# Kernel optimization log

Measured on AMD Instinct MI355X. Metric: run time of the kernel, lower is better.

The kernel has to match this reference:

```python
import jax, jax.numpy as jnp
import numpy as np
from jax import lax

FAULT_RATE = 0.1


def _quant_inject(key, x, num_faults):
    # scale/zero-point quantization to [0,255] (matches compute_scale_zero_point)
    mn, mx = x.min(), x.max()
    scale = (mx - mn) / 255.0
    zp = jnp.clip(-mn / scale, 0.0, 255.0)
    q = jnp.clip(jnp.round(zp + x / scale), 0.0, 255.0)
    if num_faults > 0:
        # vectorized equivalent of the serial fault loop: pick unique indices,
        # each consumes a random 1..8 fault budget; faulted bytes are zeroed
        # (the original loop sets tensor_bits = 0).
        n = q.size
        m = min(num_faults, n)  # each index consumes >= 1 fault
        k1, k2 = jax.random.split(key)
        cand = jax.random.permutation(k1, n)[:m]  # without replacement
        sizes = jax.random.randint(k2, (m,), 1, 9)
        prefix = jnp.cumsum(sizes) - sizes  # budget consumed before each pick
        keep = prefix < num_faults
        qf = q.reshape(-1)
        qf = qf.at[cand].set(jnp.where(keep, jnp.zeros((), q.dtype), qf[cand]))
        q = qf.reshape(q.shape)
    return scale * (q - zp)


def _conv(x, w, b):
    y = lax.conv_general_dilated(x, w, (1, 1), 'VALID',
                                 dimension_numbers=('NCHW', 'OIHW', 'NCHW'))
    return y + b[None, :, None, None]


def _maxpool(x):
    return lax.reduce_window(x, -np.inf, lax.max, (1, 1, 2, 2), (1, 1, 2, 2), 'VALID')


def _fault_schedule(total_activation_count):
    total_faults = int(total_activation_count * 8 * FAULT_RATE)
    rng = np.random.default_rng(0)
    return [int(v) for v in rng.multinomial(total_faults, np.ones(4) / 4)]


def _forward(x, conv1_w, conv1_b, conv2_w, conv2_b, fc_w, fc_b,
             fc1_w, fc1_b, fc2_w, fc2_b, fpl):
    ks = jax.random.split(jax.random.key(42), 11)
    x = _conv(x, conv1_w, conv1_b)
    x = _quant_inject(ks[0], x, 0)
    x = jax.nn.relu(x)
    x = _quant_inject(ks[1], x, fpl[0])
    x = _maxpool(x)
    x = _quant_inject(ks[2], x, 0)
    x = _conv(x, conv2_w, conv2_b)
    x = _quant_inject(ks[3], x, 0)
    x = jax.nn.relu(x)
    x = _quant_inject(ks[4], x, fpl[1])
    x = _maxpool(x)
    x = _quant_inject(ks[5], x, 0)
    x = x.reshape(x.shape[0], -1)  # [B, 400]
    x = x @ fc_w.T + fc_b
    x = _quant_inject(ks[6], x, 0)
    x = jax.nn.relu(x)
    x = _quant_inject(ks[7], x, fpl[2])
    x = x @ fc1_w.T + fc1_b
    x = _quant_inject(ks[8], x, 0)
    x = jax.nn.relu(x)
    x = _quant_inject(ks[9], x, fpl[3])
    x = x @ fc2_w.T + fc2_b
    x = _quant_inject(ks[10], x, 0)
    return jax.nn.log_softmax(x, axis=1)


def setup_inputs() -> dict:
    key = jax.random.key(0)
    ks = jax.random.split(key, 11)
    B = 8192
    return {
        'x': jax.random.normal(ks[0], (B, 1, 32, 32), jnp.float32),
        'conv1_w': jax.random.normal(ks[1], (6, 1, 5, 5), jnp.float32) * 0.2,
        'conv1_b': jax.random.normal(ks[2], (6,), jnp.float32) * 0.1,
        'conv2_w': jax.random.normal(ks[3], (16, 6, 5, 5), jnp.float32) * 0.08,
        'conv2_b': jax.random.normal(ks[4], (16,), jnp.float32) * 0.1,
        'fc_w': jax.random.normal(ks[5], (120, 400), jnp.float32) * 0.05,
        'fc_b': jax.random.normal(ks[6], (120,), jnp.float32) * 0.1,
        'fc1_w': jax.random.normal(ks[7], (84, 120), jnp.float32) * 0.09,
        'fc1_b': jax.random.normal(ks[8], (84,), jnp.float32) * 0.1,
        'fc2_w': jax.random.normal(ks[9], (10, 84), jnp.float32) * 0.1,
        'fc2_b': jax.random.normal(ks[10], (10,), jnp.float32) * 0.1,
        'total_activation_count': 833024,
    }


def reference(x, conv1_w, conv1_b, conv2_w, conv2_b, fc_w, fc_b,
              fc1_w, fc1_b, fc2_w, fc2_b, total_activation_count):
    fpl = _fault_schedule(total_activation_count)
    return _forward(x, conv1_w, conv1_b, conv2_w, conv2_b, fc_w, fc_b,
                    fc1_w, fc1_b, fc2_w, fc2_b, fpl)
```

## Files before the change

kernel.cpp:

```cpp
#include <hip/hip_runtime.h>
#include <cstdint>
#include <cstring>
#include <cmath>
#include <cstdlib>
#include <vector>
#include <thread>
#include <mutex>
#include <algorithm>

#define JAX_PARTITIONABLE 1


static inline uint32_t rotl32(uint32_t v, int d) { return (v << d) | (v >> (32 - d)); }

static inline void tf2x32(uint32_t k0, uint32_t k1, uint32_t c0, uint32_t c1,
                          uint32_t& o0, uint32_t& o1) {
  uint32_t ks0 = k0, ks1 = k1, ks2 = k0 ^ k1 ^ 0x1BD11BDAu;
  uint32_t ks[3] = {ks0, ks1, ks2};
  uint32_t x0 = c0 + ks0, x1 = c1 + ks1;
  static const int R[2][4] = {{13, 15, 26, 6}, {17, 29, 16, 24}};
  for (int g = 0; g < 5; g++) {
    const int* r = R[g & 1];
    for (int q = 0; q < 4; q++) { x0 += x1; x1 = rotl32(x1, r[q]); x1 ^= x0; }
    x0 += ks[(g + 1) % 3];
    x1 += ks[(g + 2) % 3] + (uint32_t)(g + 1);
  }
  o0 = x0; o1 = x1;
}

static void jax_split(const uint32_t key[2], int num, uint32_t (*out)[2]) {
#if JAX_PARTITIONABLE
  for (int i = 0; i < num; i++)
    tf2x32(key[0], key[1], 0u, (uint32_t)i, out[i][0], out[i][1]);
#else
  std::vector<uint32_t> o(2 * (size_t)num);
  for (int i = 0; i < num; i++) {
    uint32_t a, b;
    tf2x32(key[0], key[1], (uint32_t)i, (uint32_t)(num + i), a, b);
    o[i] = a; o[num + i] = b;
  }
  for (int i = 0; i < num; i++) { out[i][0] = o[2 * i]; out[i][1] = o[2 * i + 1]; }
#endif
}

static inline uint32_t jax_bits32_at(const uint32_t key[2], uint64_t n_total, uint64_t i) {
#if JAX_PARTITIONABLE
  uint32_t b0, b1;
  tf2x32(key[0], key[1], (uint32_t)(i >> 32), (uint32_t)i, b0, b1);
  return b0 ^ b1;
#else
  uint64_t half = (n_total + 1) / 2;
  uint64_t pi = (i < half) ? i : (i - half);
  uint32_t c1 = (half + pi < n_total) ? (uint32_t)(half + pi) : 0u;
  uint32_t b0, b1;
  tf2x32(key[0], key[1], (uint32_t)pi, c1, b0, b1);
  return (i < half) ? b0 : b1;
#endif
}

static void seedseq_zero_state(uint64_t out[4]) {
  const uint32_t INIT_A = 0x43b0d7e5u, MULT_A = 0x931e8875u;
  const uint32_t INIT_B = 0x8b51f9ddu, MULT_B = 0x58f38dedu;
  uint32_t pool[4];
  uint32_t hc = INIT_A;
  auto hashmix = [&](uint32_t v) -> uint32_t {
    v ^= hc; hc *= MULT_A; v *= hc; v ^= v >> 16; return v;
  };
  auto mixf = [](uint32_t x, uint32_t y) -> uint32_t {
    uint32_t r = x * 0xca01f9ddu - y * 0x4973f715u;
    r ^= r >> 16; return r;
  };
  uint32_t entropy0 = 0u;
  for (int i = 0; i < 4; i++) pool[i] = hashmix(i < 1 ? entropy0 : 0u);
  for (int s = 0; s < 4; s++)
    for (int d = 0; d < 4; d++)
      if (s != d) pool[d] = mixf(pool[d], hashmix(pool[s]));
  uint32_t st[8];
  uint32_t hc2 = INIT_B;
  int cyc = 0;
  for (int i = 0; i < 8; i++) {
    uint32_t v = pool[cyc]; cyc = (cyc + 1) & 3;
    v ^= hc2; hc2 *= MULT_B; v *= hc2; v ^= v >> 16;
    st[i] = v;
  }
  for (int k = 0; k < 4; k++)
    out[k] = (uint64_t)st[2 * k] | ((uint64_t)st[2 * k + 1] << 32);
}

struct PCG64 {
  __uint128_t state, inc;
  explicit PCG64(const uint64_t s[4]) {
    __uint128_t initstate = (((__uint128_t)s[0]) << 64) | s[1];
    __uint128_t initseq = (((__uint128_t)s[2]) << 64) | s[3];
    state = 0; inc = (initseq << 1) | 1;
    step(); state += initstate; step();
  }
  void step() {
    const __uint128_t MUL =
        (((__uint128_t)0x2360ed051fc65da4ULL) << 64) | 0x4385df649fccf645ULL;
    state = state * MUL + inc;
  }
  uint64_t next64() {
    step();
    uint64_t hi = (uint64_t)(state >> 64), lo = (uint64_t)state;
    uint64_t x = hi ^ lo;
    unsigned rot = (unsigned)(state >> 122);
    return (x >> rot) | (x << ((64u - rot) & 63u));
  }
  double nextd() { return (double)(next64() >> 11) * (1.0 / 9007199254740992.0); }
};

static int64_t binomial_inversion(PCG64& st, int64_t n, double p) {
  double q = 1.0 - p;
  double qn = std::exp(n * std::log(q));
  double np_ = n * p;
  int64_t bound = (int64_t)std::min((double)n, np_ + 10.0 * std::sqrt(np_ * q + 1));
  int64_t X = 0;
  double px = qn;
  double U = st.nextd();
  while (U > px) {
    X++;
    if (X > bound) { X = 0; px = qn; U = st.nextd(); }
    else { U -= px; px = ((n - X + 1) * p * px) / (X * q); }
  }
  return X;
}

static int64_t random_binomial_btpe(PCG64& st, int64_t n, double p) {
  double r, q, fm, p1, xm, xl, xr, c, laml, lamr, p2, p3, p4;
  double a, u, v, s, F, rho, t, A, nrq, x1, x2, f1, f2, z, z2, w, w2, x;
  int64_t m, y, k, i;
  r = std::min(p, 1.0 - p);
  q = 1.0 - r;
  fm = n * r + r;
  m = (int64_t)std::floor(fm);
  p1 = std::floor(2.195 * std::sqrt(n * r * q) - 4.6 * q) + 0.5;
  xm = m + 0.5;
  xl = xm - p1;
  xr = xm + p1;
  c = 0.134 + 20.5 / (15.3 + m);
  a = (fm - xl) / (fm - xl * r);
  laml = a * (1.0 + a / 2.0);
  a = (xr - fm) / (xr * q);
  lamr = a * (1.0 + a / 2.0);
  p2 = p1 * (1.0 + 2.0 * c);
  p3 = p2 + c / laml;
  p4 = p3 + c / lamr;

Step10:
  nrq = n * r * q;
  u = st.nextd() * p4;
  v = st.nextd();
  if (u > p1) goto Step20;
  y = (int64_t)std::floor(xm - p1 * v + u);
  goto Step60;
Step20:
  if (u > p2) goto Step30;
  x = xl + (u - p1) / c;
  v = v * c + 1.0 - std::fabs(m - x + 0.5) / p1;
  if (v > 1.0) goto Step10;
  y = (int64_t)std::floor(x);
  goto Step50;
Step30:
  if (u > p3) goto Step40;
  y = (int64_t)std::floor(xl + std::log(v) / laml);
  if ((y < 0) || (v == 0.0)) goto Step10;
  v = v * (u - p2) * laml;
  goto Step50;
Step40:
  y = (int64_t)std::floor(xr - std::log(v) / lamr);
  if ((y > n) || (v == 0.0)) goto Step10;
  v = v * (u - p3) * lamr;
  goto Step50;
Step50:
  k = (y > m) ? (y - m) : (m - y);
  if ((k > 20) && (k < (nrq / 2.0 - 1))) goto Step52;
  s = r / q;
  a = s * (n + 1);
  F = 1.0;
  if (m < y) { for (i = m + 1; i <= y; i++) F *= (a / i - s); }
  else if (m > y) { for (i = y + 1; i <= m; i++) F /= (a / i - s); }
  if (v > F) goto Step10;
  goto Step60;
Step52:
  rho = ((double)k / nrq) * ((k * (k / 3.0 + 0.625) + 0.16666666666666666) / nrq + 0.5);
  t = -((double)k) * k / (2 * nrq);
  A = std::log(v);
  if (A < (t - rho)) goto Step60;
  if (A > (t + rho)) goto Step10;
  x1 = (double)(y + 1);
  f1 = (double)(m + 1);
  z = (double)(n + 1 - m);
  w = (double)(n - y + 1);
  x2 = x1 * x1; f2 = f1 * f1; z2 = z * z; w2 = w * w;
  if (A > (xm * std::log(f1 / x1) + (n - m + 0.5) * std::log(z / w) +
           (y - m) * std::log(w * r / (x1 * q)) +
           (13680. - (462. - (132. - (99. - 140. / f2) / f2) / f2) / f2) / f1 / 166320. +
           (13680. - (462. - (132. - (99. - 140. / z2) / z2) / z2) / z2) / z / 166320. +
           (13680. - (462. - (132. - (99. - 140. / x2) / x2) / x2) / x2) / x1 / 166320. +
           (13680. - (462. - (132. - (99. - 140. / w2) / w2) / w2) / w2) / w / 166320.)) {
    goto Step10;
  }
Step60:
  if (p > 0.5) y = n - y;
  return y;
}

static int64_t random_binomial(PCG64& st, double p, int64_t n) {
  if (n == 0 || p == 0.0) return 0;
  if (p <= 0.5) {
    if (p * n <= 30.0) return binomial_inversion(st, n, p);
    return random_binomial_btpe(st, n, p);
  } else {
    double q = 1.0 - p;
    if (q * n <= 30.0) return n - binomial_inversion(st, n, q);
    return n - random_binomial_btpe(st, n, q);
  }
}

static void np_multinomial4(int64_t n, int64_t out[4]) {
  uint64_t ss[4];
  seedseq_zero_state(ss);
  PCG64 st(ss);
  double pix[4] = {0.25, 0.25, 0.25, 0.25};
  double remaining_p = 1.0;
  int64_t dn = n;
  out[0] = out[1] = out[2] = out[3] = 0;
  for (int j = 0; j < 3; j++) {
    out[j] = random_binomial(st, pix[j] / remaining_p, dn);
    dn -= out[j];
    if (dn <= 0) break;
    remaining_p -= pix[j];
  }
  if (dn > 0) out[3] = dn;
}

template <typename F>
static void pfor(size_t n, int T, const F& f) {
  if (n == 0) return;
  size_t chunk = (n + (size_t)T - 1) / (size_t)T;
  std::vector<std::thread> ths;
  for (int t = 0; t < T; t++) {
    size_t lo = (size_t)t * chunk;
    if (lo >= n) break;
    size_t hi = std::min(n, lo + chunk);
    ths.emplace_back([&f, lo, hi, t]() { f(lo, hi, t); });
  }
  for (auto& th : ths) th.join();
}

static void radix_pass16(const uint32_t* kin, const uint32_t* vin, uint32_t* kout,
                         uint32_t* vout, size_t n, int shift, int T,
                         std::vector<uint32_t>& hist) {
  const size_t BN = 65536;
  hist.assign((size_t)T * BN, 0u);
  pfor(n, T, [&](size_t lo, size_t hi, int t) {
    uint32_t* h = &hist[(size_t)t * BN];
    for (size_t i = lo; i < hi; i++) h[(kin[i] >> shift) & 0xFFFFu]++;
  });
  uint32_t sum = 0;
  for (size_t d = 0; d < BN; d++)
    for (int t = 0; t < T; t++) {
      uint32_t& hc = hist[(size_t)t * BN + d];
      uint32_t cnt = hc; hc = sum; sum += cnt;
    }
  pfor(n, T, [&](size_t lo, size_t hi, int t) {
    uint32_t* h = &hist[(size_t)t * BN];
    for (size_t i = lo; i < hi; i++) {
      uint32_t d = (kin[i] >> shift) & 0xFFFFu;
      uint32_t pos = h[d]++;
      kout[pos] = kin[i]; vout[pos] = vin[i];
    }
  });
}

static void shuffle_prefix(const uint32_t key[2], uint64_t n, uint32_t J,
                           uint32_t* out, int T) {
  if (J == 0) return;
  double nn = (double)(n < 1 ? 1 : n);
  int rounds = (int)std::ceil(3.0 * std::log(nn) / std::log(4294967295.0));
  size_t N = (size_t)n;
  std::vector<uint32_t> kbuf(N), vbuf(N), kt(N), vt(N);
  std::vector<uint32_t> hist;
  pfor(N, T, [&](size_t lo, size_t hi, int) {
    for (size_t i = lo; i < hi; i++) vbuf[i] = (uint32_t)i;
  });
  uint32_t cur[2] = {key[0], key[1]};
  for (int rd = 0; rd < rounds; rd++) {
    uint32_t ch[2][2];
    jax_split(cur, 2, ch);
    cur[0] = ch[0][0]; cur[1] = ch[0][1];
    uint32_t sk[2] = {ch[1][0], ch[1][1]};
#if JAX_PARTITIONABLE
    pfor(N, T, [&](size_t lo, size_t hi, int) {
      for (size_t i = lo; i < hi; i++) {
        uint32_t b0, b1;
        tf2x32(sk[0], sk[1], (uint32_t)(i >> 32), (uint32_t)i, b0, b1);
        kbuf[i] = b0 ^ b1;
      }
    });
#else
    {
      size_t half = (N + 1) / 2;
      pfor(half, T, [&](size_t lo, size_t hi, int) {
        for (size_t i = lo; i < hi; i++) {
          uint32_t c1v = (half + i < N) ? (uint32_t)(half + i) : 0u;
          uint32_t b0, b1;
          tf2x32(sk[0], sk[1], (uint32_t)i, c1v, b0, b1);
          kbuf[i] = b0;
          if (half + i < N) kbuf[half + i] = b1;
        }
      });
    }
#endif
    radix_pass16(kbuf.data(), vbuf.data(), kt.data(), vt.data(), N, 0, T, hist);
    radix_pass16(kt.data(), vt.data(), kbuf.data(), vbuf.data(), N, 16, T, hist);
  }
  for (uint32_t j = 0; j < J; j++) out[j] = vbuf[j];
  std::sort(out, out + J);
}


static uint32_t h_faults[4 * 65536];
static uint32_t h_blob[64 + 4 * 65536];
static int h_J[4] = {0, 0, 0, 0};
static int h_off[4] = {0, 0, 0, 0};
static int h_tot = 0;
static uint64_t h_tables_B = 0;

static void compute_fault_tables(uint64_t B, int Jout[4]) {
  int T = (int)std::thread::hardware_concurrency();
  if (T < 1) T = 1;
  if (T > 48) T = 48;
  int64_t fpl[4];
  np_multinomial4((int64_t)(833024ull * 8ull / 10ull), fpl);
  uint32_t k42[2] = {0u, 42u};
  uint32_t ks[11][2];
  jax_split(k42, 11, ks);
  const int kidx[4] = {1, 4, 7, 9};
  const uint64_t ns[4] = {B * 4704u, B * 1600u, B * 120u, B * 84u};
  for (int L = 0; L < 4; L++) {
    uint32_t ch[2][2];
    jax_split(ks[kidx[L]], 2, ch);
    uint32_t rc[2][2];
    jax_split(ch[1], 2, rc);
    int64_t nf = fpl[L];
    uint64_t m = ((uint64_t)nf < ns[L]) ? (uint64_t)nf : ns[L];
    int64_t csum = 0;
    uint32_t J = 0;
    for (uint64_t j = 0; j < m; j++) {
      if (csum >= nf) break;
      J++;
      csum += 1 + (int64_t)(jax_bits32_at(rc[1], m, j) & 7u);
    }
    if (J > 65536u) J = 65536u;
    shuffle_prefix(ch[0], ns[L], J, &h_faults[(size_t)L * 65536], T);
    Jout[L] = (int)J;
  }
  memset(h_blob, 0, 256);
  for (int s = 0; s < 11; s++) { h_blob[2 * s] = 0xFFFFFFFFu; h_blob[2 * s + 1] = 0u; }
  int tot = 0;
  for (int L = 0; L < 4; L++) {
    h_off[L] = tot;
    memcpy(h_blob + 64 + tot, h_faults + (size_t)L * 65536, (size_t)Jout[L] * 4);
    tot += Jout[L];
  }
  h_tot = tot;
}

namespace {
struct FaultTableInit {
  FaultTableInit() {
    compute_fault_tables(8192ull, h_J);
    h_tables_B = 8192ull;
  }
};
FaultTableInit g_fault_table_init;
std::mutex g_table_mu;
}


#define INF_F __builtin_inff()

__device__ __forceinline__ uint32_t f_to_mono(float f) {
  uint32_t u = __float_as_uint(f);
  return (u & 0x80000000u) ? ~u : (u | 0x80000000u);
}
__device__ __forceinline__ float mono_to_f(uint32_t m) {
  uint32_t u = (m & 0x80000000u) ? (m & 0x7FFFFFFFu) : ~m;
  return __uint_as_float(u);
}

struct QP { float scale; float zp; };

__device__ __forceinline__ QP qp_make(float mn, float mx) {
  QP p;
  p.scale = (mx - mn) / 255.0f;
  p.zp = fminf(fmaxf((-mn) / p.scale, 0.0f), 255.0f);
  return p;
}
__device__ __forceinline__ QP qp_load(const uint32_t* stats, int s) {
  return qp_make(mono_to_f(stats[2 * s + 0]), mono_to_f(stats[2 * s + 1]));
}
__device__ __forceinline__ float quant_apply(float x, QP p) {
  float q = rintf(p.zp + x / p.scale);
  q = fminf(fmaxf(q, 0.0f), 255.0f);
  return p.scale * (q - p.zp);
}
__device__ __forceinline__ float quant_zero(QP p) { return p.scale * (0.0f - p.zp); }
__device__ __forceinline__ int q_idx(float x, QP p) {
  float q = rintf(p.zp + x / p.scale);
  q = fminf(fmaxf(q, 0.0f), 255.0f);
  return (int)q;
}

__device__ __forceinline__ QP qp_derive_relu(const uint32_t* stats, int s, QP qa) {
  float mn = mono_to_f(stats[2 * s + 0]);
  float mx = mono_to_f(stats[2 * s + 1]);
  float dmn = fmaxf(quant_apply(mn, qa), 0.0f);
  float dmx = fmaxf(quant_apply(mx, qa), 0.0f);
  return qp_make(dmn, dmx);
}

__device__ __forceinline__ void block_minmax(float lmn, float lmx, uint32_t* mn_slot,
                                             uint32_t* mx_slot) {
  for (int off = 32; off > 0; off >>= 1) {
    lmn = fminf(lmn, __shfl_down(lmn, off, 64));
    lmx = fmaxf(lmx, __shfl_down(lmx, off, 64));
  }
  __shared__ float wmn[16], wmx[16];
  int wid = threadIdx.x >> 6, lane = threadIdx.x & 63;
  int nw = (blockDim.x + 63) >> 6;
  if (lane == 0) { wmn[wid] = lmn; wmx[wid] = lmx; }
  __syncthreads();
  if (threadIdx.x == 0) {
    float m0 = wmn[0], m1 = wmx[0];
    for (int i = 1; i < nw; i++) { m0 = fminf(m0, wmn[i]); m1 = fmaxf(m1, wmx[i]); }
    atomicMin(mn_slot, f_to_mono(m0));
    atomicMax(mx_slot, f_to_mono(m1));
  }
}

__device__ __forceinline__ int lowb(const uint32_t* a, int n, uint32_t v) {
  int lo = 0, hi = n;
  while (lo < hi) {
    int mid = (lo + hi) >> 1;
    if (a[mid] < v) lo = mid + 1; else hi = mid;
  }
  return lo;
}


template <int IMG>
__device__ __forceinline__ void stage_img(const float* __restrict__ x, float* s_img,
                                          int ib0, int B) {
  for (int i = threadIdx.x; i < IMG * 256; i += 256) {
    int im = i >> 8, k = i & 255;
    if (ib0 + im < B) {
      float4 v = ((const float4*)(x + (size_t)(ib0 + im) * 1024))[k];
      int row = k >> 3, c4 = k & 7;
      ((float4*)s_img)[im * 288 + row * 9 + c4] = v;
    }
  }
}

__device__ __forceinline__ void stage_w1(const float* __restrict__ w, float* s_w) {
  if (threadIdx.x < 168) {
    int c = threadIdx.x / 28, f = threadIdx.x - c * 28;
    s_w[threadIdx.x] = (f < 25) ? w[c * 25 + f] : 0.0f;
  }
}

template <int O>
__device__ __forceinline__ void conv1_rowpair(const float* __restrict__ img, int r0,
                                              int colbase, const float* wr,
                                              float acc0[14], float acc1[14]) {
#pragma unroll
  for (int ir = 0; ir < 6; ir++) {
    float f[20];
    const float* rp = img + (r0 + ir) * 36 + colbase;
#pragma unroll
    for (int k = 0; k < 5; k++) *(float4*)&f[4 * k] = *(const float4*)&rp[4 * k];
    if (ir < 5) {
#pragma unroll
      for (int j = 0; j < 5; j++)
#pragma unroll
        for (int cc = 0; cc < 14; cc++)
          acc0[cc] = fmaf(f[O + cc + j], wr[ir * 5 + j], acc0[cc]);
    }
    if (ir >= 1) {
#pragma unroll
      for (int j = 0; j < 5; j++)
#pragma unroll
        for (int cc = 0; cc < 14; cc++)
          acc1[cc] = fmaf(f[O + cc + j], wr[(ir - 1) * 5 + j], acc1[cc]);
    }
  }
}

__global__ __launch_bounds__(256) void k_conv1_mat(const float* __restrict__ x,
    const float* __restrict__ w, const float* __restrict__ b,
    float* __restrict__ raw, uint32_t* __restrict__ stats, int B) {
  __shared__ __align__(16) float s_img[4 * 1152];
  __shared__ __align__(16) float s_w[168];
  __shared__ float s_b[8];
  int ib0 = blockIdx.x * 4;
  stage_img<4>(x, s_img, ib0, B);
  stage_w1(w, s_w);
  if (threadIdx.x < 6) s_b[threadIdx.x] = b[threadIdx.x];
  __syncthreads();
  float lmn = INF_F, lmx = -INF_F;
#pragma unroll 1
  for (int task = threadIdx.x; task < 4 * 168; task += 256) {
    int im = task / 168, rem = task - im * 168;
    if (ib0 + im >= B) continue;
    int c = rem / 28, r2 = rem - c * 28, pr = r2 >> 1, h = r2 & 1;
    float wr[25];
#pragma unroll
    for (int k = 0; k < 25; k++) wr[k] = s_w[c * 28 + k];
    float bias = s_b[c];
    float acc0[14], acc1[14];
#pragma unroll
    for (int cc = 0; cc < 14; cc++) { acc0[cc] = bias; acc1[cc] = bias; }
    const float* img = &s_img[im * 1152];
    if (h == 0) conv1_rowpair<0>(img, 2 * pr, 0, wr, acc0, acc1);
    else        conv1_rowpair<2>(img, 2 * pr, 12, wr, acc0, acc1);
    float* d0 = raw + (size_t)(ib0 + im) * 4704 + c * 784 + (2 * pr) * 28 + h * 14;
    float* d1 = d0 + 28;
#pragma unroll
    for (int q = 0; q < 7; q++) {
      float2 v0; v0.x = acc0[2 * q]; v0.y = acc0[2 * q + 1];
      float2 v1; v1.x = acc1[2 * q]; v1.y = acc1[2 * q + 1];
      *(float2*)&d0[2 * q] = v0;
      *(float2*)&d1[2 * q] = v1;
    }
#pragma unroll
    for (int cc = 0; cc < 14; cc++) {
      lmn = fminf(lmn, fminf(acc0[cc], acc1[cc]));
      lmx = fmaxf(lmx, fmaxf(acc0[cc], acc1[cc]));
    }
  }
  block_minmax(lmn, lmx, &stats[0], &stats[1]);
}

__global__ __launch_bounds__(256) void k_pool1(const float* __restrict__ raw,
    uint32_t* __restrict__ stats, const uint32_t* __restrict__ faults, int J,
    float* __restrict__ p1, int B) {
  __shared__ float s_K[256];
  __shared__ uint32_t s_fl[64];
  __shared__ int s_lo, s_nf;
  QP q0 = qp_load(stats, 0);
  QP qB = qp_derive_relu(stats, 0, q0);
  {
    int i = threadIdx.x;
    float a = fmaxf(q0.scale * ((float)i - q0.zp), 0.0f);
    float kq = rintf(qB.zp + a / qB.scale);
    s_K[i] = fminf(fmaxf(kq, 0.0f), 255.0f);
  }
  int T0 = blockIdx.x * 256;
  if (threadIdx.x == 0) {
    int im0 = T0 / 84;
    int imL = (T0 + 255) / 84;
    uint32_t lo32 = (uint32_t)im0 * 4704u;
    uint32_t hi32 = (uint32_t)(imL + 1) * 4704u;
    int lo = lowb(faults, J, lo32);
    s_lo = lo; s_nf = lowb(faults, J, hi32) - lo;
  }
  __syncthreads();
  int nf = s_nf, flo = s_lo;
  for (int i = threadIdx.x; i < nf && i < 64; i += 256) s_fl[i] = faults[flo + i];
  __syncthreads();
  const uint32_t* farr = (nf <= 64) ? s_fl : (faults + flo);

  float lmn = INF_F, lmx = -INF_F;
  int T = T0 + threadIdx.x;
  if (T < B * 84) {
    int im = T / 84, rem = T - im * 84;
    int c = rem / 14, pr = rem - c * 14;
    uint32_t e0 = (uint32_t)im * 4704u + (uint32_t)(c * 784 + 2 * pr * 28);
    const float* src = raw + (size_t)im * 4704 + c * 784 + (2 * pr) * 28;
    float k0[28], k1[28];
#pragma unroll
    for (int q = 0; q < 7; q++) {
      float4 v = *(const float4*)&src[4 * q];
      k0[4 * q + 0] = s_K[q_idx(v.x, q0)];
      k0[4 * q + 1] = s_K[q_idx(v.y, q0)];
      k0[4 * q + 2] = s_K[q_idx(v.z, q0)];
      k0[4 * q + 3] = s_K[q_idx(v.w, q0)];
    }
#pragma unroll
    for (int q = 0; q < 7; q++) {
      float4 v = *(const float4*)&src[28 + 4 * q];
      k1[4 * q + 0] = s_K[q_idx(v.x, q0)];
      k1[4 * q + 1] = s_K[q_idx(v.y, q0)];
      k1[4 * q + 2] = s_K[q_idx(v.z, q0)];
      k1[4 * q + 3] = s_K[q_idx(v.w, q0)];
    }
    if (nf > 0) {
      int a = lowb(farr, nf, e0);
      while (a < nf) {
        uint32_t g = farr[a];
        if (g >= e0 + 56u) break;
        int d = (int)(g - e0);
#pragma unroll
        for (int cc = 0; cc < 28; cc++) {
          if (cc == d) k0[cc] = 0.0f;
          if (cc + 28 == d) k1[cc] = 0.0f;
        }
        a++;
      }
    }
    float* dst = p1 + (size_t)im * 1176 + c * 196 + pr * 14;
#pragma unroll
    for (int q = 0; q < 7; q++) {
      float ka = fmaxf(fmaxf(k0[4 * q], k0[4 * q + 1]), fmaxf(k1[4 * q], k1[4 * q + 1]));
      float kb = fmaxf(fmaxf(k0[4 * q + 2], k0[4 * q + 3]),
                       fmaxf(k1[4 * q + 2], k1[4 * q + 3]));
      float2 v;
      v.x = qB.scale * (ka - qB.zp);
      v.y = qB.scale * (kb - qB.zp);
      *(float2*)&dst[2 * q] = v;
      lmn = fminf(lmn, fminf(v.x, v.y));
      lmx = fmaxf(lmx, fmaxf(v.x, v.y));
    }
  }
  block_minmax(lmn, lmx, &stats[4], &stats[5]);
}

__global__ __launch_bounds__(256) void k_conv2(const float* __restrict__ p1,
    const float* __restrict__ w, const float* __restrict__ b,
    float* __restrict__ raw, uint32_t* __restrict__ stats, int B) {
  __shared__ __align__(16) float s_in[8 * 1680];
  __shared__ __align__(16) float s_w[16 * 6 * 28];
  __shared__ float s_b[16];
  int ib0 = blockIdx.x * 8;
  QP q2 = qp_load(stats, 2);
  for (int i = threadIdx.x; i < 8 * 1176; i += 256) {
    int im = i / 1176, rem = i - im * 1176;
    if (ib0 + im < B) {
      int ci = rem / 196, r2 = rem - ci * 196;
      int rr = r2 / 14, cc = r2 - rr * 14;
      float v = quant_apply(p1[(size_t)(ib0 + im) * 1176 + rem], q2);
      s_in[im * 1680 + ci * 280 + rr * 20 + cc] = v;
    }
  }
  for (int i = threadIdx.x; i < 2688; i += 256) {
    int fi = i / 28, f = i - fi * 28;
    s_w[i] = (f < 25) ? w[fi * 25 + f] : 0.0f;
  }
  if (threadIdx.x < 16) s_b[threadIdx.x] = b[threadIdx.x];
  __syncthreads();
  float lmn = INF_F, lmx = -INF_F;
#pragma unroll 1
  for (int task = threadIdx.x; task < 640; task += 256) {
    int im = task / 80, rem = task - im * 80;
    if (ib0 + im >= B) continue;
    int c2p = rem / 10, r = rem - c2p * 10;
    int cA = 2 * c2p, cB = 2 * c2p + 1;
    float accA[10], accB[10];
    float bA = s_b[cA], bB = s_b[cB];
#pragma unroll
    for (int cc = 0; cc < 10; cc++) { accA[cc] = bA; accB[cc] = bB; }
    const float* inb = &s_in[im * 1680];
#pragma unroll 1
    for (int ci = 0; ci < 6; ci++) {
      float wrA[28], wrB[28];
#pragma unroll
      for (int k = 0; k < 7; k++) {
        *(float4*)&wrA[4 * k] = *(const float4*)&s_w[(cA * 6 + ci) * 28 + 4 * k];
        *(float4*)&wrB[4 * k] = *(const float4*)&s_w[(cB * 6 + ci) * 28 + 4 * k];
      }
      const float* cb = inb + ci * 280;
#pragma unroll
      for (int i = 0; i < 5; i++) {
        float f[16];
        const float* rp = cb + (r + i) * 20;
#pragma unroll
        for (int k = 0; k < 4; k++) *(float4*)&f[4 * k] = *(const float4*)&rp[4 * k];
#pragma unroll
        for (int j = 0; j < 5; j++) {
#pragma unroll
          for (int cc = 0; cc < 10; cc++) accA[cc] = fmaf(f[cc + j], wrA[i * 5 + j], accA[cc]);
#pragma unroll
          for (int cc = 0; cc < 10; cc++) accB[cc] = fmaf(f[cc + j], wrB[i * 5 + j], accB[cc]);
        }
      }
    }
    float* rbA = raw + (size_t)(ib0 + im) * 1600 + cA * 100 + r * 10;
    float* rbB = raw + (size_t)(ib0 + im) * 1600 + cB * 100 + r * 10;
#pragma unroll
    for (int cc = 0; cc < 10; cc++) {
      rbA[cc] = accA[cc]; rbB[cc] = accB[cc];
      lmn = fminf(lmn, fminf(accA[cc], accB[cc]));
      lmx = fmaxf(lmx, fmaxf(accA[cc], accB[cc]));
    }
  }
  block_minmax(lmn, lmx, &stats[6], &stats[7]);
}

__global__ __launch_bounds__(256) void k_pool2s(const float* __restrict__ raw,
    uint32_t* __restrict__ stats, const uint32_t* __restrict__ faults, int J,
    float* __restrict__ p2, int B) {
  __shared__ float s_K[256];
  __shared__ uint32_t s_fl[64];
  __shared__ int s_lo, s_nf;
  QP q3 = qp_load(stats, 3);
  QP qE = qp_derive_relu(stats, 3, q3);
  {
    int i = threadIdx.x;
    float a = fmaxf(q3.scale * ((float)i - q3.zp), 0.0f);
    float kq = rintf(qE.zp + a / qE.scale);
    s_K[i] = fminf(fmaxf(kq, 0.0f), 255.0f);
  }
  int T0 = blockIdx.x * 256;
  if (threadIdx.x == 0) {
    int im0 = T0 / 80;
    int imL = (T0 + 255) / 80;
    uint32_t lo32 = (uint32_t)im0 * 1600u;
    uint32_t hi32 = (uint32_t)(imL + 1) * 1600u;
    int lo = lowb(faults, J, lo32);
    s_lo = lo; s_nf = lowb(faults, J, hi32) - lo;
  }
  __syncthreads();
  int nf = s_nf, flo = s_lo;
  for (int i = threadIdx.x; i < nf && i < 64; i += 256) s_fl[i] = faults[flo + i];
  __syncthreads();
  const uint32_t* farr = (nf <= 64) ? s_fl : (faults + flo);

  float lmn = INF_F, lmx = -INF_F;
  int T = T0 + threadIdx.x;
  if (T < B * 80) {
    int im = T / 80, rem = T - im * 80;
    int c = rem / 5, pr = rem - c * 5;
    uint32_t e0 = (uint32_t)im * 1600u + (uint32_t)(c * 100 + 2 * pr * 10);
    const float* src = raw + (size_t)im * 1600 + c * 100 + (2 * pr) * 10;
    float kk[20];
#pragma unroll
    for (int q = 0; q < 5; q++) {
      float4 v = *(const float4*)&src[4 * q];
      kk[4 * q + 0] = s_K[q_idx(v.x, q3)];
      kk[4 * q + 1] = s_K[q_idx(v.y, q3)];
      kk[4 * q + 2] = s_K[q_idx(v.z, q3)];
      kk[4 * q + 3] = s_K[q_idx(v.w, q3)];
    }
    if (nf > 0) {
      int a = lowb(farr, nf, e0);
      while (a < nf) {
        uint32_t g = farr[a];
        if (g >= e0 + 20u) break;
        int d = (int)(g - e0);
#pragma unroll
        for (int cc = 0; cc < 20; cc++) if (cc == d) kk[cc] = 0.0f;
        a++;
      }
    }
    float* dst = p2 + (size_t)im * 400 + c * 25 + pr * 5;
#pragma unroll
    for (int q = 0; q < 5; q++) {
      float kp = fmaxf(fmaxf(kk[2 * q], kk[2 * q + 1]),
                       fmaxf(kk[10 + 2 * q], kk[10 + 2 * q + 1]));
      float v = qE.scale * (kp - qE.zp);
      dst[q] = v;
      lmn = fminf(lmn, v); lmx = fmaxf(lmx, v);
    }
  }
  block_minmax(lmn, lmx, &stats[10], &stats[11]);
}

template <int IN, int OUT, int ROWS, int SPLIT, bool CHAIN>
__global__ __launch_bounds__(256) void k_fc(const float* __restrict__ in,
    const float* __restrict__ w, const float* __restrict__ bias,
    float* __restrict__ out, uint32_t* stats, int squant, int s_out,
    const uint32_t* __restrict__ faults, int J) {
  __shared__ __align__(16) float rows[ROWS * IN];
  int b0 = blockIdx.x * ROWS;
  QP p{1.0f, 0.0f};
  if (CHAIN) {
    QP qa = qp_load(stats, squant);
    p = qp_derive_relu(stats, squant, qa);
    for (int i = threadIdx.x; i < ROWS * IN; i += 256)
      rows[i] = quant_apply(fmaxf(quant_apply(in[(size_t)b0 * IN + i], qa), 0.0f), p);
  } else {
    p = qp_load(stats, squant);
    for (int i = threadIdx.x; i < ROWS * IN; i += 256)
      rows[i] = quant_apply(in[(size_t)b0 * IN + i], p);
  }
  if (faults) {
    __syncthreads();
    uint32_t base = (uint32_t)b0 * IN;
    int lo = lowb(faults, J, base), hi2 = lowb(faults, J, base + ROWS * IN);
    float qz = quant_zero(p);
    for (int t = lo + (int)threadIdx.x; t < hi2; t += 256) rows[faults[t] - base] = qz;
  }
  __syncthreads();
  constexpr int RP = ROWS / SPLIT;
  int o = threadIdx.x % OUT;
  int sp = threadIdx.x / OUT;
  float lmn = INF_F, lmx = -INF_F;
  if (sp < SPLIT) {
    float acc[RP];
#pragma unroll
    for (int r = 0; r < RP; r++) acc[r] = bias[o];
    const float* wr = &w[(size_t)o * IN];
    for (int k = 0; k < IN; k += 4) {
      float4 wv = *(const float4*)&wr[k];
#pragma unroll
      for (int r = 0; r < RP; r++) {
        float4 xv = *(const float4*)&rows[(sp * RP + r) * IN + k];
        acc[r] = fmaf(xv.x, wv.x, acc[r]);
        acc[r] = fmaf(xv.y, wv.y, acc[r]);
        acc[r] = fmaf(xv.z, wv.z, acc[r]);
        acc[r] = fmaf(xv.w, wv.w, acc[r]);
      }
    }
#pragma unroll
    for (int r = 0; r < RP; r++) {
      out[(size_t)(b0 + sp * RP + r) * OUT + o] = acc[r];
      lmn = fminf(lmn, acc[r]); lmx = fmaxf(lmx, acc[r]);
    }
  }
  block_minmax(lmn, lmx, &stats[2 * s_out], &stats[2 * s_out + 1]);
}

__global__ __launch_bounds__(256) void k_logsoftmax(const float* __restrict__ logits,
    float* __restrict__ out, const uint32_t* stats, int slot, int B) {
  int i = blockIdx.x * 256 + threadIdx.x;
  if (i >= B) return;
  QP p = qp_load(stats, slot);
  float v[10];
  float m = -INF_F;
#pragma unroll
  for (int k = 0; k < 10; k++) {
    v[k] = quant_apply(logits[(size_t)i * 10 + k], p);
    m = fmaxf(m, v[k]);
  }
  float s = 0.0f;
#pragma unroll
  for (int k = 0; k < 10; k++) s += expf(v[k] - m);
  float ls = logf(s);
#pragma unroll
  for (int k = 0; k < 10; k++) out[(size_t)i * 10 + k] = (v[k] - m) - ls;
}

extern "C" void kernel_launch(void* const* d_in, const int* in_sizes, int n_in,
                              void* d_out, int out_size, void* d_ws, size_t ws_size,
                              hipStream_t stream) {
  const float* x    = (const float*)d_in[0];
  const float* c1w  = (const float*)d_in[1];
  const float* c1b  = (const float*)d_in[2];
  const float* c2w  = (const float*)d_in[3];
  const float* c2b  = (const float*)d_in[4];
  const float* fcw  = (const float*)d_in[5];
  const float* fcb  = (const float*)d_in[6];
  const float* fc1w = (const float*)d_in[7];
  const float* fc1b = (const float*)d_in[8];
  const float* fc2w = (const float*)d_in[9];
  const float* fc2b = (const float*)d_in[10];
  float* out = (float*)d_out;
  const int B = in_sizes[0] / 1024;

  if ((uint64_t)B != h_tables_B) {
    std::lock_guard<std::mutex> lk(g_table_mu);
    if ((uint64_t)B != h_tables_B) {
      compute_fault_tables((uint64_t)B, h_J);
      h_tables_B = (uint64_t)B;
    }
  }

  uint8_t* ws = (uint8_t*)d_ws;
  uint32_t* stats = (uint32_t*)ws;
  uint32_t* fl = (uint32_t*)(ws + 256);
  size_t off = 256 + (size_t)4 * 65536 * sizeof(uint32_t);
  float* p1   = (float*)(ws + off); off += (size_t)B * 1176 * 4;
  float* p2   = (float*)(ws + off); off += (size_t)B * 400 * 4;
  float* h1   = (float*)(ws + off); off += (size_t)B * 120 * 4;
  float* h2   = (float*)(ws + off); off += (size_t)B * 84 * 4;
  float* lg   = (float*)(ws + off); off += (size_t)B * 10 * 4;
  float* raw2 = (float*)(ws + off); off += (size_t)B * 1600 * 4;
  float* raw1 = (float*)(ws + off); off += (size_t)B * 4704 * 4;
  if (ws_size < off) return;

  const uint32_t* f0 = fl + h_off[0];
  const uint32_t* f1 = fl + h_off[1];
  const uint32_t* f2 = fl + h_off[2];
  const uint32_t* f3 = fl + h_off[3];

  hipMemcpyAsync(ws, h_blob, 256 + (size_t)h_tot * sizeof(uint32_t),
                 hipMemcpyHostToDevice, stream);

  int g4 = (B + 3) / 4, g8 = (B + 7) / 8;

  k_conv1_mat<<<g4, 256, 0, stream>>>(x, c1w, c1b, raw1, stats, B);
  k_pool1<<<(B * 84 + 255) / 256, 256, 0, stream>>>(raw1, stats, f0, h_J[0], p1, B);

  k_conv2<<<g8, 256, 0, stream>>>(p1, c2w, c2b, raw2, stats, B);
  k_pool2s<<<(B * 80 + 255) / 256, 256, 0, stream>>>(raw2, stats, f1, h_J[1], p2, B);

  k_fc<400, 120, 16, 2, false><<<B / 16, 256, 0, stream>>>(p2, fcw, fcb, h1, stats,
                                                           5, 6, nullptr, 0);
  k_fc<120, 84, 16, 2, true><<<B / 16, 256, 0, stream>>>(h1, fc1w, fc1b, h2, stats,
                                                         6, 8, f2, h_J[2]);
  k_fc<84, 10, 32, 8, true><<<B / 32, 256, 0, stream>>>(h2, fc2w, fc2b, lg, stats,
                                                        8, 10, f3, h_J[3]);
  k_logsoftmax<<<(B + 255) / 256, 256, 0, stream>>>(lg, out, stats, 10, B);
}
```

Before: 614.1 us.

## Fuse 2x2 window max into conv1 and store only faulted windows in full

Result: no change. 623.4 us (+1.5%).

```diff
diff --git a/kernel.cpp b/kernel.cpp
--- a/kernel.cpp
+++ b/kernel.cpp
@@ -322,10 +322,11 @@
 
 
 static uint32_t h_faults[4 * 65536];
-static uint32_t h_blob[64 + 4 * 65536];
+static uint32_t h_blob[64 + 5 * 65536];
 static int h_J[4] = {0, 0, 0, 0};
 static int h_off[4] = {0, 0, 0, 0};
 static int h_tot = 0;
+static int h_nfw = 0;
 static uint64_t h_tables_B = 0;
 
 static void compute_fault_tables(uint64_t B, int Jout[4]) {
@@ -366,6 +367,21 @@
     tot += Jout[L];
   }
   h_tot = tot;
+  {
+    std::vector<uint32_t> wv;
+    wv.reserve(Jout[0]);
+    for (int j = 0; j < Jout[0]; j++) {
+      uint32_t e = h_faults[j];
+      uint32_t im = e / 4704u, rem = e - im * 4704u;
+      uint32_t c = rem / 784u, r2 = rem - c * 784u;
+      uint32_t rr = r2 / 28u, cc = r2 - rr * 28u;
+      wv.push_back(im * 1176u + c * 196u + (rr >> 1) * 14u + (cc >> 1));
+    }
+    std::sort(wv.begin(), wv.end());
+    wv.erase(std::unique(wv.begin(), wv.end()), wv.end());
+    h_nfw = (int)std::min<size_t>(wv.size(), 65536);
+    memcpy(h_blob + 64 + tot, wv.data(), (size_t)h_nfw * 4);
+  }
 }
 
 namespace {
@@ -459,7 +475,7 @@
     if (ib0 + im < B) {
       float4 v = ((const float4*)(x + (size_t)(ib0 + im) * 1024))[k];
       int row = k >> 3, c4 = k & 7;
-      ((float4*)s_img)[im * 288 + row * 9 + c4] = v;
+      ((float4*)s_img)[im * 320 + row * 10 + c4] = v;
     }
   }
 }
@@ -478,7 +494,7 @@
 #pragma unroll
   for (int ir = 0; ir < 6; ir++) {
     float f[20];
-    const float* rp = img + (r0 + ir) * 36 + colbase;
+    const float* rp = img + (r0 + ir) * 40 + colbase;
 #pragma unroll
     for (int k = 0; k < 5; k++) *(float4*)&f[4 * k] = *(const float4*)&rp[4 * k];
     if (ir < 5) {
@@ -500,15 +516,30 @@
 
 __global__ __launch_bounds__(256) void k_conv1_mat(const float* __restrict__ x,
     const float* __restrict__ w, const float* __restrict__ b,
-    float* __restrict__ raw, uint32_t* __restrict__ stats, int B) {
-  __shared__ __align__(16) float s_img[4 * 1152];
+    float* __restrict__ wmax, float* __restrict__ side,
+    const uint32_t* __restrict__ fw, int nfw_g,
+    uint32_t* __restrict__ stats, int B) {
+  __shared__ __align__(16) float s_img[4 * 1280];
   __shared__ __align__(16) float s_w[168];
   __shared__ float s_b[8];
+  __shared__ uint32_t s_fw[64];
+  __shared__ int s_flo, s_fn;
   int ib0 = blockIdx.x * 4;
   stage_img<4>(x, s_img, ib0, B);
   stage_w1(w, s_w);
   if (threadIdx.x < 6) s_b[threadIdx.x] = b[threadIdx.x];
+  if (threadIdx.x == 0) {
+    uint32_t w0 = (uint32_t)ib0 * 1176u;
+    uint32_t w1 = (uint32_t)(ib0 + 4) * 1176u;
+    int lo = lowb(fw, nfw_g, w0);
+    s_flo = lo; s_fn = lowb(fw, nfw_g, w1) - lo;
+  }
   __syncthreads();
+  int fn = s_fn, flo = s_flo;
+  for (int i = threadIdx.x; i < fn && i < 64; i += 256) s_fw[i] = fw[flo + i];
+  __syncthreads();
+  const uint32_t* fwa = (fn <= 64) ? s_fw : (fw + flo);
+
   float lmn = INF_F, lmx = -INF_F;
 #pragma unroll 1
   for (int task = threadIdx.x; task < 4 * 168; task += 256) {
@@ -522,17 +553,33 @@
     float acc0[14], acc1[14];
 #pragma unroll
     for (int cc = 0; cc < 14; cc++) { acc0[cc] = bias; acc1[cc] = bias; }
-    const float* img = &s_img[im * 1152];
+    const float* img = &s_img[im * 1280];
     if (h == 0) conv1_rowpair<0>(img, 2 * pr, 0, wr, acc0, acc1);
     else        conv1_rowpair<2>(img, 2 * pr, 12, wr, acc0, acc1);
-    float* d0 = raw + (size_t)(ib0 + im) * 4704 + c * 784 + (2 * pr) * 28 + h * 14;
-    float* d1 = d0 + 28;
-#pragma unroll
-    for (int q = 0; q < 7; q++) {
-      float2 v0; v0.x = acc0[2 * q]; v0.y = acc0[2 * q + 1];
-      float2 v1; v1.x = acc1[2 * q]; v1.y = acc1[2 * q + 1];
-      *(float2*)&d0[2 * q] = v0;
-      *(float2*)&d1[2 * q] = v1;
+    uint32_t wid0 = (uint32_t)(ib0 + im) * 1176u + (uint32_t)(c * 196 + pr * 14 + h * 7);
+    float* dst = wmax + wid0;
+#pragma unroll
+    for (int k = 0; k < 7; k++) {
+      float wm = fmaxf(fmaxf(acc0[2 * k], acc0[2 * k + 1]),
+                       fmaxf(acc1[2 * k], acc1[2 * k + 1]));
+      dst[k] = wm;
+    }
+    if (fn > 0) {
+      int a = lowb(fwa, fn, wid0);
+      while (a < fn) {
+        uint32_t wg = fwa[a];
+        if (wg >= wid0 + 7u) break;
+#pragma unroll
+        for (int k = 0; k < 7; k++) {
+          if ((int)(wg - wid0) == k) {
+            float4 sv;
+            sv.x = acc0[2 * k]; sv.y = acc0[2 * k + 1];
+            sv.z = acc1[2 * k]; sv.w = acc1[2 * k + 1];
+            *(float4*)&side[4 * (flo + a)] = sv;
+          }
+        }
+        a++;
+      }
     }
 #pragma unroll
     for (int cc = 0; cc < 14; cc++) {
@@ -543,85 +590,85 @@
   block_minmax(lmn, lmx, &stats[0], &stats[1]);
 }
 
-__global__ __launch_bounds__(256) void k_pool1(const float* __restrict__ raw,
-    uint32_t* __restrict__ stats, const uint32_t* __restrict__ faults, int J,
-    float* __restrict__ p1, int B) {
-  __shared__ float s_K[256];
-  __shared__ uint32_t s_fl[64];
-  __shared__ int s_lo, s_nf;
+__global__ __launch_bounds__(256) void k_pool1(const float* __restrict__ wmax,
+    const float* __restrict__ side, const uint32_t* __restrict__ fw, int nfw_g,
+    const uint32_t* __restrict__ faults, int J,
+    uint32_t* __restrict__ stats, float* __restrict__ p1, int B) {
+  __shared__ float s_V[256];
+  __shared__ uint32_t s_fw[64], s_fl[64];
+  __shared__ int s_wlo, s_wn, s_elo, s_en;
   QP q0 = qp_load(stats, 0);
   QP qB = qp_derive_relu(stats, 0, q0);
   {
     int i = threadIdx.x;
     float a = fmaxf(q0.scale * ((float)i - q0.zp), 0.0f);
-    float kq = rintf(qB.zp + a / qB.scale);
-    s_K[i] = fminf(fmaxf(kq, 0.0f), 255.0f);
+    float kq = fminf(fmaxf(rintf(qB.zp + a / qB.scale), 0.0f), 255.0f);
+    s_V[i] = qB.scale * (kq - qB.zp);
   }
   int T0 = blockIdx.x * 256;
   if (threadIdx.x == 0) {
-    int im0 = T0 / 84;
-    int imL = (T0 + 255) / 84;
-    uint32_t lo32 = (uint32_t)im0 * 4704u;
-    uint32_t hi32 = (uint32_t)(imL + 1) * 4704u;
-    int lo = lowb(faults, J, lo32);
-    s_lo = lo; s_nf = lowb(faults, J, hi32) - lo;
+    int im0 = T0 / 84, imL = (T0 + 255) / 84;
+    uint32_t w0 = (uint32_t)im0 * 1176u, w1 = (uint32_t)(imL + 1) * 1176u;
+    int lo = lowb(fw, nfw_g, w0);
+    s_wlo = lo; s_wn = lowb(fw, nfw_g, w1) - lo;
+    uint32_t e0 = (uint32_t)im0 * 4704u, e1 = (uint32_t)(imL + 1) * 4704u;
+    int lo2 = lowb(faults, J, e0);
+    s_elo = lo2; s_en = lowb(faults, J, e1) - lo2;
   }
   __syncthreads();
-  int nf = s_nf, flo = s_lo;
-  for (int i = threadIdx.x; i < nf && i < 64; i += 256) s_fl[i] = faults[flo + i];
+  int wn = s_wn, wlo = s_wlo, en = s_en, elo = s_elo;
+  for (int i = threadIdx.x; i < wn && i < 64; i += 256) s_fw[i] = fw[wlo + i];
+  for (int i = threadIdx.x; i < en && i < 64; i += 256) s_fl[i] = faults[elo + i];
   __syncthreads();
-  const uint32_t* farr = (nf <= 64) ? s_fl : (faults + flo);
+  const uint32_t* fwa = (wn <= 64) ? s_fw : (fw + wlo);
+  const uint32_t* fla = (en <= 64) ? s_fl : (faults + elo);
 
   float lmn = INF_F, lmx = -INF_F;
   int T = T0 + threadIdx.x;
   if (T < B * 84) {
     int im = T / 84, rem = T - im * 84;
     int c = rem / 14, pr = rem - c * 14;
-    uint32_t e0 = (uint32_t)im * 4704u + (uint32_t)(c * 784 + 2 * pr * 28);
-    const float* src = raw + (size_t)im * 4704 + c * 784 + (2 * pr) * 28;
-    float k0[28], k1[28];
+    uint32_t rb = (uint32_t)im * 1176u + (uint32_t)(c * 196 + pr * 14);
+    const float* src = wmax + rb;
+    float v[14];
 #pragma unroll
     for (int q = 0; q < 7; q++) {
-      float4 v = *(const float4*)&src[4 * q];
-      k0[4 * q + 0] = s_K[q_idx(v.x, q0)];
-      k0[4 * q + 1] = s_K[q_idx(v.y, q0)];
-      k0[4 * q + 2] = s_K[q_idx(v.z, q0)];
-      k0[4 * q + 3] = s_K[q_idx(v.w, q0)];
-    }
-#pragma unroll
-    for (int q = 0; q < 7; q++) {
-      float4 v = *(const float4*)&src[28 + 4 * q];
-      k1[4 * q + 0] = s_K[q_idx(v.x, q0)];
-      k1[4 * q + 1] = s_K[q_idx(v.y, q0)];
-      k1[4 * q + 2] = s_K[q_idx(v.z, q0)];
-      k1[4 * q + 3] = s_K[q_idx(v.w, q0)];
-    }
-    if (nf > 0) {
-      int a = lowb(farr, nf, e0);
-      while (a < nf) {
-        uint32_t g = farr[a];
-        if (g >= e0 + 56u) break;
-        int d = (int)(g - e0);
-#pragma unroll
-        for (int cc = 0; cc < 28; cc++) {
-          if (cc == d) k0[cc] = 0.0f;
-          if (cc + 28 == d) k1[cc] = 0.0f;
-        }
+      float2 wm = *(const float2*)&src[2 * q];
+      v[2 * q]     = s_V[q_idx(wm.x, q0)];
+      v[2 * q + 1] = s_V[q_idx(wm.y, q0)];
+    }
+    if (wn > 0) {
+      int a = lowb(fwa, wn, rb);
+      while (a < wn) {
+        uint32_t wg = fwa[a];
+        if (wg >= rb + 14u) break;
+        int wc = (int)(wg - rb);
+        float4 sv = *(const float4*)&side[4 * (wlo + a)];
+        uint32_t eb = (uint32_t)im * 4704u + (uint32_t)(c * 784 + 2 * pr * 28 + 2 * wc);
+        float m0, mm = 0.0f;
+        int p2_;
+        p2_ = lowb(fla, en, eb);       m0 = (p2_ < en && fla[p2_] == eb)       ? 0.0f : (float)q_idx(sv.x, q0);
+        mm = fmaxf(mm * 0.0f, m0);
+        p2_ = lowb(fla, en, eb + 1u);  m0 = (p2_ < en && fla[p2_] == eb + 1u)  ? 0.0f : (float)q_idx(sv.y, q0);
+        mm = fmaxf(mm, m0);
+        p2_ = lowb(fla, en, eb + 28u); m0 = (p2_ < en && fla[p2_] == eb + 28u) ? 0.0f : (float)q_idx(sv.z, q0);
+        mm = fmaxf(mm, m0);
+        p2_ = lowb(fla, en, eb + 29u); m0 = (p2_ < en && fla[p2_] == eb + 29u) ? 0.0f : (float)q_idx(sv.w, q0);
+        mm = fmaxf(mm, m0);
+        float aa = fmaxf(q0.scale * (mm - q0.zp), 0.0f);
+        float kq = fminf(fmaxf(rintf(qB.zp + aa / qB.scale), 0.0f), 255.0f);
+#pragma unroll
+        for (int k = 0; k < 14; k++) if (k == wc) v[k] = qB.scale * (kq - qB.zp);
         a++;
       }
     }
-    float* dst = p1 + (size_t)im * 1176 + c * 196 + pr * 14;
+    float* dst = p1 + rb;
 #pragma unroll
     for (int q = 0; q < 7; q++) {
-      float ka = fmaxf(fmaxf(k0[4 * q], k0[4 * q + 1]), fmaxf(k1[4 * q], k1[4 * q + 1]));
-      float kb = fmaxf(fmaxf(k0[4 * q + 2], k0[4 * q + 3]),
-                       fmaxf(k1[4 * q + 2], k1[4 * q + 3]));
-      float2 v;
-      v.x = qB.scale * (ka - qB.zp);
-      v.y = qB.scale * (kb - qB.zp);
-      *(float2*)&dst[2 * q] = v;
-      lmn = fminf(lmn, fminf(v.x, v.y));
-      lmx = fmaxf(lmx, fmaxf(v.x, v.y));
+      float2 o; o.x = v[2 * q]; o.y = v[2 * q + 1];
+      *(float2*)&dst[2 * q] = o;
+      lmn = fminf(lmn, fminf(o.x, o.y));
+      lmx = fmaxf(lmx, fmaxf(o.x, o.y));
     }
   }
   block_minmax(lmn, lmx, &stats[4], &stats[5]);
@@ -870,28 +917,31 @@
   uint8_t* ws = (uint8_t*)d_ws;
   uint32_t* stats = (uint32_t*)ws;
   uint32_t* fl = (uint32_t*)(ws + 256);
-  size_t off = 256 + (size_t)4 * 65536 * sizeof(uint32_t);
+  size_t off = 256 + (size_t)5 * 65536 * sizeof(uint32_t);
   float* p1   = (float*)(ws + off); off += (size_t)B * 1176 * 4;
   float* p2   = (float*)(ws + off); off += (size_t)B * 400 * 4;
   float* h1   = (float*)(ws + off); off += (size_t)B * 120 * 4;
   float* h2   = (float*)(ws + off); off += (size_t)B * 84 * 4;
   float* lg   = (float*)(ws + off); off += (size_t)B * 10 * 4;
   float* raw2 = (float*)(ws + off); off += (size_t)B * 1600 * 4;
-  float* raw1 = (float*)(ws + off); off += (size_t)B * 4704 * 4;
+  float* wmax = (float*)(ws + off); off += (size_t)B * 1176 * 4;
+  float* side = (float*)(ws + off); off += (size_t)65536 * 16;
   if (ws_size < off) return;
 
   const uint32_t* f0 = fl + h_off[0];
   const uint32_t* f1 = fl + h_off[1];
   const uint32_t* f2 = fl + h_off[2];
   const uint32_t* f3 = fl + h_off[3];
-
-  hipMemcpyAsync(ws, h_blob, 256 + (size_t)h_tot * sizeof(uint32_t),
+  const uint32_t* fw = fl + h_tot;
+
+  hipMemcpyAsync(ws, h_blob, 256 + (size_t)(h_tot + h_nfw) * sizeof(uint32_t),
                  hipMemcpyHostToDevice, stream);
 
   int g4 = (B + 3) / 4, g8 = (B + 7) / 8;
 
-  k_conv1_mat<<<g4, 256, 0, stream>>>(x, c1w, c1b, raw1, stats, B);
-  k_pool1<<<(B * 84 + 255) / 256, 256, 0, stream>>>(raw1, stats, f0, h_J[0], p1, B);
+  k_conv1_mat<<<g4, 256, 0, stream>>>(x, c1w, c1b, wmax, side, fw, h_nfw, stats, B);
+  k_pool1<<<(B * 84 + 255) / 256, 256, 0, stream>>>(wmax, side, fw, h_nfw,
+                                                    f0, h_J[0], stats, p1, B);
 
   k_conv2<<<g8, 256, 0, stream>>>(p1, c2w, c2b, raw2, stats, B);
   k_pool2s<<<(B * 80 + 255) / 256, 256, 0, stream>>>(raw2, stats, f1, h_J[1], p2, B);
```
